# Optimization experiments

Hardware: AMD Instinct MI355X
Metric: run time of the kernel (lower is better)

The kernel has to match this reference:

```python
import jax, jax.numpy as jnp
import numpy as np

B, E, L, H = 4, 1024, 2048, 16
DH = E // H
SCALE = E ** -0.5  # note: original scales by embedding_dim**-0.5, not head_dim**-0.5


def setup_inputs() -> dict:
    key = jax.random.key(0)
    k1, k2, k3 = jax.random.split(key, 3)
    x = jax.random.normal(k1, (B, E, L), dtype=jnp.float32)
    # Linear init: randn(d_in, d_out) / d_in
    W_qkv = jax.random.normal(k2, (E, E), dtype=jnp.float32) / E
    W_proj = jax.random.normal(k3, (E, E), dtype=jnp.float32) / E
    b_proj = jnp.zeros((E,), dtype=jnp.float32)
    return {"x": x, "W_qkv": W_qkv, "W_proj": W_proj, "b_proj": b_proj}


def reference(x, W_qkv, W_proj, b_proj):
    b, e, l = x.shape
    # shared Q=K=V projection (channels-first Linear: (x^T @ M)^T)
    kqv = jnp.einsum('bel,ef->bfl', x, W_qkv)            # [B, E, L]
    kqv = kqv.reshape(b, H, DH, l)                        # [B, H, Dh, L]
    # scores[b,h,i,j] = <kqv[...,i], kqv[...,j]> over head dim
    scores = jnp.einsum('bhdi,bhdj->bhij', kqv, kqv)      # [B, H, L, L]
    # mask strictly-lower triangle (i > j), then scale; softmax over query axis (-2)
    mask = jnp.tril(jnp.ones((l, l), dtype=bool), k=-1)
    scores = jnp.where(mask, -jnp.inf, scores * SCALE)
    att = jax.nn.softmax(scores, axis=-2)                 # normalize over i (rows)
    # t[...,d,j] = sum_i kqv[...,d,i] * att[...,i,j]
    t = jnp.einsum('bhdi,bhij->bhdj', kqv, att).reshape(b, e, l)
    # output projection with bias (dropout is identity in eval)
    out = jnp.einsum('bel,ef->bfl', t, W_proj) + b_proj[None, :, None]
    return out
```

## Files before the change

### kernel.cpp

```cpp
#include <hip/hip_runtime.h>
#include <stdint.h>
#include <math.h>

#define B_ 4
#define E_ 1024
#define L_ 2048
#define H_ 16
#define DH_ 64
#define SCALE_ 0.03125f

typedef __bf16 bf16;
typedef __bf16 bf16x8 __attribute__((ext_vector_type(8)));
typedef __bf16 bf16x4 __attribute__((ext_vector_type(4)));
typedef float f32x4 __attribute__((ext_vector_type(4)));

__device__ __forceinline__ f32x4 mfma16(bf16x8 a, bf16x8 b, f32x4 c) {
  return __builtin_amdgcn_mfma_f32_16x16x32_bf16(a, b, c, 0, 0, 0);
}

__device__ __forceinline__ void gl_lds16(const void* g, void* lds) {
  auto* lp = reinterpret_cast<__attribute__((address_space(3))) unsigned int*>(
      reinterpret_cast<uintptr_t>(lds));
  const auto* gp = reinterpret_cast<const __attribute__((address_space(1))) unsigned int*>(
      reinterpret_cast<uintptr_t>(g));
  __builtin_amdgcn_global_load_lds(gp, lp, 16, 0, 0);
}

__global__ __launch_bounds__(256) void tconv(const float* __restrict__ in,
                                             bf16* __restrict__ out, int R, int C) {
  in  += (size_t)blockIdx.z * R * C;
  out += (size_t)blockIdx.z * R * C;
  __shared__ float t[32][33];
  const int r0 = blockIdx.x * 32, c0 = blockIdx.y * 32;
  const int lx = threadIdx.x & 31, ly = threadIdx.x >> 5;
#pragma unroll
  for (int q = 0; q < 4; q++)
    t[ly + q * 8][lx] = in[(size_t)(r0 + ly + q * 8) * C + c0 + lx];
  __syncthreads();
#pragma unroll
  for (int q = 0; q < 4; q++) {
    int c = ly + q * 8;
    out[(size_t)(c0 + c) * R + r0 + lx] = (bf16)t[lx][c];
  }
}

template <int EPI>
__global__ __launch_bounds__(256) void gemm_bt(const bf16* __restrict__ A,
                                               const bf16* __restrict__ Bt,
                                               bf16* __restrict__ outT,
                                               bf16* __restrict__ outD,
                                               float* __restrict__ outF,
                                               const float* __restrict__ bias) {
  constexpr int M = E_, N = L_, K = E_;
  const int bm = blockIdx.x, bn = blockIdx.y, b = blockIdx.z;
  __shared__ bf16 As[128 * 32];
  __shared__ bf16 Bs[128 * 32];
  const int tid = threadIdx.x, w = tid >> 6, l = tid & 63;
  const int wm = (w >> 1) << 6, wn = (w & 1) << 6;
  const bf16* Ap = A + (size_t)bm * 128 * K;
  const bf16* Bp = Bt + (size_t)b * N * K + (size_t)bn * 128 * K;
  f32x4 acc[4][4] = {};
  const int g0 = (w * 2 + 0) * 64 + l, g1 = (w * 2 + 1) * 64 + l;
  const int r0 = g0 >> 2, s0 = (g0 & 3) ^ ((r0 >> 1) & 3);
  const int r1 = g1 >> 2, s1 = (g1 & 3) ^ ((r1 >> 1) & 3);
#pragma unroll 1
  for (int kt = 0; kt < K; kt += 32) {
    __syncthreads();
    gl_lds16(Ap + (size_t)r0 * K + kt + s0 * 8, As + g0 * 8);
    gl_lds16(Ap + (size_t)r1 * K + kt + s1 * 8, As + g1 * 8);
    gl_lds16(Bp + (size_t)r0 * K + kt + s0 * 8, Bs + g0 * 8);
    gl_lds16(Bp + (size_t)r1 * K + kt + s1 * 8, Bs + g1 * 8);
    asm volatile("s_waitcnt vmcnt(0)" ::: "memory");
    __syncthreads();
    bf16x8 af[4], bfr[4];
#pragma unroll
    for (int fm = 0; fm < 4; fm++) {
      int row = wm + fm * 16 + (l & 15);
      int gg = row * 4 + ((l >> 4) ^ ((row >> 1) & 3));
      af[fm] = *(const bf16x8*)(As + gg * 8);
    }
#pragma unroll
    for (int fn = 0; fn < 4; fn++) {
      int row = wn + fn * 16 + (l & 15);
      int gg = row * 4 + ((l >> 4) ^ ((row >> 1) & 3));
      bfr[fn] = *(const bf16x8*)(Bs + gg * 8);
    }
#pragma unroll
    for (int fm = 0; fm < 4; fm++)
#pragma unroll
      for (int fn = 0; fn < 4; fn++)
        acc[fm][fn] = mfma16(af[fm], bfr[fn], acc[fm][fn]);
  }
  const int cm = bm * 128 + wm, cn = bn * 128 + wn;
  if (EPI == 0) {
#pragma unroll
    for (int fn = 0; fn < 4; fn++) {
#pragma unroll
      for (int fm = 0; fm < 4; fm++) {
        int n = cn + fn * 16 + (l & 15);
        int m = cm + fm * 16 + ((l >> 4) << 2);
        f32x4 v = acc[fm][fn];
        bf16x4 pv = {(bf16)v[0], (bf16)v[1], (bf16)v[2], (bf16)v[3]};
        *(bf16x4*)(outT + (size_t)b * N * M + (size_t)n * M + m) = pv;
#pragma unroll
        for (int r = 0; r < 4; r++)
          outD[(size_t)b * M * N + (size_t)(m + r) * N + n] = pv[r];
      }
    }
  } else {
#pragma unroll
    for (int fm = 0; fm < 4; fm++) {
      int m = cm + fm * 16 + ((l >> 4) << 2);
#pragma unroll
      for (int r = 0; r < 4; r++) {
        float bv = bias[m + r];
#pragma unroll
        for (int fn = 0; fn < 4; fn++) {
          int n = cn + fn * 16 + (l & 15);
          outF[(size_t)b * M * N + (size_t)(m + r) * N + n] = acc[fm][fn][r] + bv;
        }
      }
    }
  }
}

__global__ __launch_bounds__(512) void attn(const bf16* __restrict__ kqvT,
                                            const bf16* __restrict__ kqvD,
                                            bf16* __restrict__ tT) {
  const int linear = (int)blockIdx.x + 16 * ((int)blockIdx.y + 16 * (int)blockIdx.z);
  const int qb = 15 - (linear >> 6);
  const int h = linear & 15, b = (linear >> 4) & 3;
  const int tid = threadIdx.x, w = tid >> 6, l = tid & 63;
  const int j0 = qb * 128 + w * 16;
  __shared__ bf16 Ks[2][64 * 64];
  __shared__ bf16 Vs[2][64 * 64];
  __shared__ bf16 Ps[8][16 * 64];
  const size_t bT = (size_t)b * L_ * E_;
  const size_t bD = (size_t)b * E_ * L_;
  bf16x8 qa[2];
  {
    size_t qoff = bT + (size_t)(j0 + (l & 15)) * E_ + h * 64 + ((l >> 4) << 3);
    qa[0] = *(const bf16x8*)(kqvT + qoff);
    qa[1] = *(const bf16x8*)(kqvT + qoff + 32);
#pragma unroll
    for (int e = 0; e < 8; e++) {
      qa[0][e] = (bf16)((float)qa[0][e] * SCALE_);
      qa[1][e] = (bf16)((float)qa[1][e] * SCALE_);
    }
  }
  float mrun[4] = {0.f, 0.f, 0.f, 0.f};
  float lsum[4] = {0.f, 0.f, 0.f, 0.f};
  f32x4 tacc[4] = {};
  bf16* myPs = &Ps[w][0];
  const int g = w * 64 + l;
  const int rS = g >> 3, sS = (g & 7) ^ (rS & 7);
  const int nch = 2 * (qb + 1);

#define STAGE(c, buf)                                                                  \
  do {                                                                                 \
    const int i0_ = (c) * 64;                                                          \
    gl_lds16(kqvT + bT + (size_t)(i0_ + rS) * E_ + h * 64 + sS * 8, &Ks[buf][g * 8]);  \
    gl_lds16(kqvD + bD + (size_t)(h * 64 + rS) * L_ + i0_ + sS * 8, &Vs[buf][g * 8]);  \
  } while (0)

  STAGE(0, 0);
  asm volatile("s_waitcnt vmcnt(0)" ::: "memory");
  __syncthreads();

#pragma unroll 1
  for (int c = 0; c < nch; c++) {
    const int cur = c & 1;
    if (c + 1 < nch) STAGE(c + 1, cur ^ 1);
    const int i0 = c * 64;
    const bf16* Kc = &Ks[cur][0];
    const bf16* Vc = &Vs[cur][0];
    if (i0 <= j0 + 15) {
      f32x4 sacc[4];
      __builtin_amdgcn_s_setprio(1);
#pragma unroll
      for (int fi = 0; fi < 4; fi++) {
        int row = fi * 16 + (l & 15);
        bf16x8 k0 = *(const bf16x8*)(Kc + row * 64 + (((l >> 4) ^ (row & 7)) << 3));
        bf16x8 k1 = *(const bf16x8*)(Kc + row * 64 + ((((l >> 4) + 4) ^ (row & 7)) << 3));
        f32x4 z = {};
        z = mfma16(qa[0], k0, z);
        z = mfma16(qa[1], k1, z);
        sacc[fi] = z;
      }
      __builtin_amdgcn_s_setprio(0);
      const int jrb = j0 + ((l >> 4) << 2);
      if (i0 + 63 > j0) {
#pragma unroll
        for (int fi = 0; fi < 4; fi++) {
          int i = i0 + fi * 16 + (l & 15);
#pragma unroll
          for (int r = 0; r < 4; r++)
            if (i > jrb + r) sacc[fi][r] = -INFINITY;
        }
      }
      bool ov = false;
#pragma unroll
      for (int fi = 0; fi < 4; fi++)
#pragma unroll
        for (int r = 0; r < 4; r++) ov |= (sacc[fi][r] > mrun[r] + 8.f);
      if (__any(ov)) {
        float mx[4];
#pragma unroll
        for (int r = 0; r < 4; r++)
          mx[r] = fmaxf(fmaxf(sacc[0][r], sacc[1][r]), fmaxf(sacc[2][r], sacc[3][r]));
#pragma unroll
        for (int r = 0; r < 4; r++) {
          mx[r] = fmaxf(mx[r], __shfl_xor(mx[r], 1));
          mx[r] = fmaxf(mx[r], __shfl_xor(mx[r], 2));
          mx[r] = fmaxf(mx[r], __shfl_xor(mx[r], 4));
          mx[r] = fmaxf(mx[r], __shfl_xor(mx[r], 8));
        }
#pragma unroll
        for (int r = 0; r < 4; r++) {
          float mn = fmaxf(mrun[r], mx[r]);
          float a = __expf(mrun[r] - mn);
          lsum[r] *= a;
#pragma unroll
          for (int fd = 0; fd < 4; fd++) tacc[fd][r] *= a;
          mrun[r] = mn;
        }
      }
#pragma unroll
      for (int fi = 0; fi < 4; fi++) {
        int icol = fi * 16 + (l & 15);
#pragma unroll
        for (int r = 0; r < 4; r++) {
          float p = __expf(sacc[fi][r] - mrun[r]);
          lsum[r] += p;
          int jl = ((l >> 4) << 2) + r;
          int slot = (icol >> 3) ^ (jl & 7);
          myPs[jl * 64 + slot * 8 + (icol & 7)] = (bf16)p;
        }
      }
      bf16x8 pa[2];
      {
        int jl = l & 15;
#pragma unroll
        for (int kc = 0; kc < 2; kc++)
          pa[kc] = *(const bf16x8*)(myPs + jl * 64 + (((kc * 4 + (l >> 4)) ^ (jl & 7)) << 3));
      }
      __builtin_amdgcn_s_setprio(1);
#pragma unroll
      for (int fd = 0; fd < 4; fd++) {
        int row = fd * 16 + (l & 15);
#pragma unroll
        for (int kc = 0; kc < 2; kc++) {
          bf16x8 vf = *(const bf16x8*)(Vc + row * 64 + (((kc * 4 + (l >> 4)) ^ (row & 7)) << 3));
          tacc[fd] = mfma16(pa[kc], vf, tacc[fd]);
        }
      }
      __builtin_amdgcn_s_setprio(0);
    }
    asm volatile("s_waitcnt vmcnt(0)" ::: "memory");
    __syncthreads();
  }
#undef STAGE
#pragma unroll
  for (int r = 0; r < 4; r++) {
    lsum[r] += __shfl_xor(lsum[r], 1);
    lsum[r] += __shfl_xor(lsum[r], 2);
    lsum[r] += __shfl_xor(lsum[r], 4);
    lsum[r] += __shfl_xor(lsum[r], 8);
  }
#pragma unroll
  for (int r = 0; r < 4; r++) {
    int j = j0 + ((l >> 4) << 2) + r;
    float inv = 1.0f / lsum[r];
#pragma unroll
    for (int fd = 0; fd < 4; fd++) {
      int d = fd * 16 + (l & 15);
      tT[bT + (size_t)j * E_ + h * 64 + d] = (bf16)(tacc[fd][r] * inv);
    }
  }
}

extern "C" void kernel_launch(void* const* d_in, const int* in_sizes, int n_in,
                              void* d_out, int out_size, void* d_ws, size_t ws_size,
                              hipStream_t stream) {
  const float* x     = (const float*)d_in[0];
  const float* Wqkv  = (const float*)d_in[1];
  const float* Wproj = (const float*)d_in[2];
  const float* bias  = (const float*)d_in[3];
  float* out = (float*)d_out;
  char* ws = (char*)d_ws;
  bf16* Wt_qkv  = (bf16*)ws;
  bf16* Wt_proj = (bf16*)(ws + (2ull << 20));
  bf16* xT      = (bf16*)(ws + (4ull << 20));
  bf16* kqvT    = (bf16*)(ws + (20ull << 20));
  bf16* kqvD    = (bf16*)(ws + (36ull << 20));
  bf16* tT      = xT;

  tconv<<<dim3(32, 32, 1), 256, 0, stream>>>(Wqkv, Wt_qkv, E_, E_);
  tconv<<<dim3(32, 32, 1), 256, 0, stream>>>(Wproj, Wt_proj, E_, E_);
  tconv<<<dim3(32, 64, B_), 256, 0, stream>>>(x, xT, E_, L_);
  gemm_bt<0><<<dim3(8, 16, B_), 256, 0, stream>>>(Wt_qkv, xT, kqvT, kqvD,
                                                  (float*)nullptr, (const float*)nullptr);
  attn<<<dim3(16, 16, B_), 512, 0, stream>>>(kqvT, kqvD, tT);
  gemm_bt<1><<<dim3(8, 16, B_), 256, 0, stream>>>(Wt_proj, tT, (bf16*)nullptr,
                                                  (bf16*)nullptr, out, bias);
}
```

Measured before the change: 228.6 us.

## Double-buffer GEMM LDS tiles and merge weight transposes into one launch

```diff
diff --git a/kernel.cpp b/kernel.cpp
--- a/kernel.cpp
+++ b/kernel.cpp
@@ -41,6 +41,26 @@
   for (int q = 0; q < 4; q++) {
     int c = ly + q * 8;
     out[(size_t)(c0 + c) * R + r0 + lx] = (bf16)t[lx][c];
+  }
+}
+
+__global__ __launch_bounds__(256) void wconv(const float* __restrict__ in0,
+                                             const float* __restrict__ in1,
+                                             bf16* __restrict__ out0,
+                                             bf16* __restrict__ out1) {
+  const float* in = blockIdx.z ? in1 : in0;
+  bf16* out = blockIdx.z ? out1 : out0;
+  __shared__ float t[32][33];
+  const int r0 = blockIdx.x * 32, c0 = blockIdx.y * 32;
+  const int lx = threadIdx.x & 31, ly = threadIdx.x >> 5;
+#pragma unroll
+  for (int q = 0; q < 4; q++)
+    t[ly + q * 8][lx] = in[(size_t)(r0 + ly + q * 8) * E_ + c0 + lx];
+  __syncthreads();
+#pragma unroll
+  for (int q = 0; q < 4; q++) {
+    int c = ly + q * 8;
+    out[(size_t)(c0 + c) * E_ + r0 + lx] = (bf16)t[lx][c];
   }
 }
 
@@ -52,9 +72,10 @@
                                                float* __restrict__ outF,
                                                const float* __restrict__ bias) {
   constexpr int M = E_, N = L_, K = E_;
+  constexpr int NIT = K / 32;
   const int bm = blockIdx.x, bn = blockIdx.y, b = blockIdx.z;
-  __shared__ bf16 As[128 * 32];
-  __shared__ bf16 Bs[128 * 32];
+  __shared__ bf16 As[2][128 * 32];
+  __shared__ bf16 Bs[2][128 * 32];
   const int tid = threadIdx.x, w = tid >> 6, l = tid & 63;
   const int wm = (w >> 1) << 6, wn = (w & 1) << 6;
   const bf16* Ap = A + (size_t)bm * 128 * K;
@@ -63,34 +84,44 @@
   const int g0 = (w * 2 + 0) * 64 + l, g1 = (w * 2 + 1) * 64 + l;
   const int r0 = g0 >> 2, s0 = (g0 & 3) ^ ((r0 >> 1) & 3);
   const int r1 = g1 >> 2, s1 = (g1 & 3) ^ ((r1 >> 1) & 3);
+
+#define STAGE_G(kt_, buf)                                              \
+  do {                                                                 \
+    gl_lds16(Ap + (size_t)r0 * K + (kt_) + s0 * 8, &As[buf][g0 * 8]);  \
+    gl_lds16(Ap + (size_t)r1 * K + (kt_) + s1 * 8, &As[buf][g1 * 8]);  \
+    gl_lds16(Bp + (size_t)r0 * K + (kt_) + s0 * 8, &Bs[buf][g0 * 8]);  \
+    gl_lds16(Bp + (size_t)r1 * K + (kt_) + s1 * 8, &Bs[buf][g1 * 8]);  \
+  } while (0)
+
+  STAGE_G(0, 0);
+  asm volatile("s_waitcnt vmcnt(0)" ::: "memory");
+  __syncthreads();
 #pragma unroll 1
-  for (int kt = 0; kt < K; kt += 32) {
-    __syncthreads();
-    gl_lds16(Ap + (size_t)r0 * K + kt + s0 * 8, As + g0 * 8);
-    gl_lds16(Ap + (size_t)r1 * K + kt + s1 * 8, As + g1 * 8);
-    gl_lds16(Bp + (size_t)r0 * K + kt + s0 * 8, Bs + g0 * 8);
-    gl_lds16(Bp + (size_t)r1 * K + kt + s1 * 8, Bs + g1 * 8);
-    asm volatile("s_waitcnt vmcnt(0)" ::: "memory");
-    __syncthreads();
+  for (int it = 0; it < NIT; it++) {
+    const int cur = it & 1;
+    if (it + 1 < NIT) STAGE_G((it + 1) * 32, cur ^ 1);
     bf16x8 af[4], bfr[4];
 #pragma unroll
     for (int fm = 0; fm < 4; fm++) {
       int row = wm + fm * 16 + (l & 15);
       int gg = row * 4 + ((l >> 4) ^ ((row >> 1) & 3));
-      af[fm] = *(const bf16x8*)(As + gg * 8);
+      af[fm] = *(const bf16x8*)(&As[cur][gg * 8]);
     }
 #pragma unroll
     for (int fn = 0; fn < 4; fn++) {
       int row = wn + fn * 16 + (l & 15);
       int gg = row * 4 + ((l >> 4) ^ ((row >> 1) & 3));
-      bfr[fn] = *(const bf16x8*)(Bs + gg * 8);
+      bfr[fn] = *(const bf16x8*)(&Bs[cur][gg * 8]);
     }
 #pragma unroll
     for (int fm = 0; fm < 4; fm++)
 #pragma unroll
       for (int fn = 0; fn < 4; fn++)
         acc[fm][fn] = mfma16(af[fm], bfr[fn], acc[fm][fn]);
-  }
+    asm volatile("s_waitcnt vmcnt(0)" ::: "memory");
+    __syncthreads();
+  }
+#undef STAGE_G
   const int cm = bm * 128 + wm, cn = bn * 128 + wn;
   if (EPI == 0) {
 #pragma unroll
@@ -295,8 +326,7 @@
   bf16* kqvD    = (bf16*)(ws + (36ull << 20));
   bf16* tT      = xT;
 
-  tconv<<<dim3(32, 32, 1), 256, 0, stream>>>(Wqkv, Wt_qkv, E_, E_);
-  tconv<<<dim3(32, 32, 1), 256, 0, stream>>>(Wproj, Wt_proj, E_, E_);
+  wconv<<<dim3(32, 32, 2), 256, 0, stream>>>(Wqkv, Wproj, Wt_qkv, Wt_proj);
   tconv<<<dim3(32, 64, B_), 256, 0, stream>>>(x, xT, E_, L_);
   gemm_bt<0><<<dim3(8, 16, B_), 256, 0, stream>>>(Wt_qkv, xT, kqvT, kqvD,
                                                   (float*)nullptr, (const float*)nullptr);
```

Result: faster. 213.0 us (-6.8%).
